# Performance work log

Hardware: AMD Instinct MI355X
Metric: run time of the kernel (lower is better)

Reference implementation:

```python
import jax, jax.numpy as jnp
import numpy as np

N, E = 50000, 800000
F_IN, HID, HEADS, NCLS = 128, 64, 4, 16
NEG_SLOPE = 0.2


def setup_inputs() -> dict:
    key = jax.random.key(0)
    ks = jax.random.split(key, 16)
    def glorot(k, shape):
        fan_in, fan_out = shape[0], shape[-1]
        lim = jnp.sqrt(6.0 / (fan_in + fan_out))
        return jax.random.uniform(k, shape, jnp.float32, -lim, lim)
    x = jax.random.normal(ks[0], (N, F_IN), jnp.float32)
    edge_index = jax.random.randint(ks[1], (2, E), 0, N, dtype=jnp.int64)
    inp = {"x": x, "edge_index": edge_index}
    # layer 1: F_IN -> HID x HEADS (concat)
    inp["W1"] = glorot(ks[2], (F_IN, HEADS * HID))
    inp["a1_src"] = glorot(ks[3], (HEADS, HID))
    inp["a1_dst"] = glorot(ks[4], (HEADS, HID))
    inp["b1"] = jnp.zeros((HEADS * HID,), jnp.float32)
    # layer 2: HEADS*HID -> HID x HEADS (concat)
    inp["W2"] = glorot(ks[5], (HEADS * HID, HEADS * HID))
    inp["a2_src"] = glorot(ks[6], (HEADS, HID))
    inp["a2_dst"] = glorot(ks[7], (HEADS, HID))
    inp["b2"] = jnp.zeros((HEADS * HID,), jnp.float32)
    # layer 3: HEADS*HID -> NCLS, heads=1, concat=False (mean)
    inp["W3"] = glorot(ks[8], (HEADS * HID, NCLS))
    inp["a3_src"] = glorot(ks[9], (1, NCLS))
    inp["a3_dst"] = glorot(ks[10], (1, NCLS))
    inp["b3"] = jnp.zeros((NCLS,), jnp.float32)
    return inp


def gat_conv(x, src, dst, W, a_src, a_dst, b, heads, out_dim, concat):
    n = x.shape[0]
    h = (x @ W).reshape(n, heads, out_dim)           # [N, H, D]
    s_src = jnp.sum(h * a_src, axis=-1)              # [N, H]
    s_dst = jnp.sum(h * a_dst, axis=-1)              # [N, H]
    e = jax.nn.leaky_relu(s_src[src] + s_dst[dst], NEG_SLOPE)  # [E, H]
    # segment softmax over incoming edges of each dst node
    m = jax.ops.segment_max(e, dst, num_segments=n)
    ex = jnp.exp(e - m[dst])
    z = jax.ops.segment_sum(ex, dst, num_segments=n)
    alpha = ex / z[dst]                              # [E, H]
    msg = h[src] * alpha[:, :, None]                 # [E, H, D]
    out = jax.ops.segment_sum(msg, dst, num_segments=n)  # [N, H, D]
    out = out.reshape(n, heads * out_dim) if concat else out.mean(axis=1)
    return out + b


def reference(x, edge_index, W1, a1_src, a1_dst, b1, W2, a2_src, a2_dst, b2,
              W3, a3_src, a3_dst, b3):
    n = x.shape[0]
    loop = jnp.arange(n, dtype=edge_index.dtype)
    src = jnp.concatenate([edge_index[0], loop])     # add self-loops (PyG default)
    dst = jnp.concatenate([edge_index[1], loop])
    h = jax.nn.elu(gat_conv(x, src, dst, W1, a1_src, a1_dst, b1, HEADS, HID, True))
    h = jax.nn.elu(gat_conv(h, src, dst, W2, a2_src, a2_dst, b2, HEADS, HID, True))
    h = gat_conv(h, src, dst, W3, a3_src, a3_dst, b3, 1, NCLS, False)
    return jax.nn.log_softmax(h, axis=1)
```

## Files before the change

kernel.cpp:

```cpp
#include <hip/hip_runtime.h>
#include <hip/hip_bf16.h>
#include <math.h>

#define N_NODES 50000
#define N_EDGES 800000
#define F_IN    128
#define HID     64
#define HEADS   4
#define NCLS    16
#define NEG_SLOPE 0.2f

typedef __attribute__((ext_vector_type(8))) _Float16 half8v;
typedef __attribute__((ext_vector_type(4))) float f32x4;
typedef __attribute__((ext_vector_type(2))) float f32x2;

static __device__ __forceinline__ float lrelu(float x) {
    return x >= 0.f ? x : NEG_SLOPE * x;
}
static __device__ __forceinline__ unsigned short f2h(float f) {
    _Float16 h = (_Float16)f;
    return __builtin_bit_cast(unsigned short, h);
}
static __device__ __forceinline__ float h2f(unsigned short u) {
    return (float)__builtin_bit_cast(_Float16, u);
}

__global__ void k_zero(int4* __restrict__ p, int n4) {
    int i = blockIdx.x * blockDim.x + threadIdx.x;
    if (i < n4) p[i] = int4{0, 0, 0, 0};
}

#define NB_WT1  128
#define NB_WT2  256
#define NB_HIST 3125
__global__ void k_prep(const float* __restrict__ W1, unsigned short* __restrict__ W1t,
                       const float* __restrict__ W2, unsigned short* __restrict__ W2t,
                       const int* __restrict__ dst, int* __restrict__ counts,
                       unsigned short* __restrict__ rank) {
    int bid = blockIdx.x, tid = threadIdx.x;
    if (bid < NB_WT1) {
        int i = bid * 256 + tid;
        int k = i >> 8, c = i & 255;
        W1t[c * F_IN + k] = f2h(W1[i]);
    } else if (bid < NB_WT1 + NB_WT2) {
        int i = (bid - NB_WT1) * 256 + tid;
        int k = i >> 8, c = i & 255;
        W2t[c * 256 + k] = f2h(W2[i]);
    } else {
        int i = (bid - NB_WT1 - NB_WT2) * 256 + tid;
        if (i < N_EDGES) rank[i] = (unsigned short)atomicAdd(&counts[dst[i]], 1);
    }
}

__global__ __launch_bounds__(256) void k_scan1(const int* __restrict__ counts, int* __restrict__ incl,
                                               int* __restrict__ bsums, int n) {
    __shared__ int wsum[4];
    int blk = blockIdx.x, tid = threadIdx.x;
    int lane = tid & 63, w = tid >> 6;
    int i0 = blk * 1024 + tid * 4;
    int v[4];
    #pragma unroll
    for (int j = 0; j < 4; j++) v[j] = (i0 + j < n) ? counts[i0 + j] : 0;
    int t = v[0] + v[1] + v[2] + v[3];
    int x = t;
    #pragma unroll
    for (int d = 1; d < 64; d <<= 1) { int y = __shfl_up(x, d); if (lane >= d) x += y; }
    if (lane == 63) wsum[w] = x;
    __syncthreads();
    int woff = 0;
    #pragma unroll
    for (int ww = 0; ww < 4; ww++) woff += (ww < w) ? wsum[ww] : 0;
    int p = woff + x - t;
    #pragma unroll
    for (int j = 0; j < 4; j++) { p += v[j]; if (i0 + j < n) incl[i0 + j] = p; }
    if (tid == 255) bsums[blk] = woff + x;
}

__global__ void k_scan2(const int* __restrict__ bsums, int* __restrict__ boffs, int nb, int* rowptr_end) {
    int lane = threadIdx.x;
    int v = (lane < nb) ? bsums[lane] : 0;
    int x = v;
    #pragma unroll
    for (int d = 1; d < 64; d <<= 1) { int y = __shfl_up(x, d); if (lane >= d) x += y; }
    if (lane < nb) boffs[lane] = x - v;
    if (lane == 63) *rowptr_end = x;
}

__global__ void k_scan3(const int* __restrict__ incl, const int* __restrict__ counts,
                        const int* __restrict__ boffs, int* __restrict__ rowptr, int n) {
    int i = blockIdx.x * blockDim.x + threadIdx.x;
    if (i < n) rowptr[i] = boffs[i >> 10] + incl[i] - counts[i];
}

static __device__ __forceinline__ int swz(int r, int lc) {
    return r * 4 + (lc ^ (r & 3) ^ ((r >> 2) & 1));
}

template<int CONVA>
static __device__ __forceinline__ void gemm_body(
        int bid, const void* __restrict__ Av, const unsigned short* __restrict__ Bt,
        const float* __restrict__ asrc, const float* __restrict__ adst,
        unsigned char* __restrict__ C8, float* __restrict__ s_src, float* __restrict__ s_dst,
        int M, int K, unsigned short* Asm, unsigned short* Bsm) {
    int tid = threadIdx.x;
    int lane = tid & 63, wid = tid >> 6;
    int bx = bid & 1, by = bid >> 1;
    int row0 = by * 128, col0 = bx * 128;
    int wr = wid >> 1, wc = wid & 1;
    f32x4 acc[4][4] = {};

    for (int k0 = 0; k0 < K; k0 += 32) {
        __syncthreads();
        #pragma unroll
        for (int s = 0; s < 2; s++) {
            int c = tid + s * 256;
            int row = c >> 2, lc = c & 3;
            int gr = row0 + row; if (gr >= M) gr = 0;
            uint4 va;
            if (CONVA) {
                const float* Af = (const float*)Av + (size_t)gr * K + k0 + lc * 8;
                float4 fa = *(const float4*)Af;
                float4 fb = *(const float4*)(Af + 4);
                va.x = (unsigned)f2h(fa.x) | ((unsigned)f2h(fa.y) << 16);
                va.y = (unsigned)f2h(fa.z) | ((unsigned)f2h(fa.w) << 16);
                va.z = (unsigned)f2h(fb.x) | ((unsigned)f2h(fb.y) << 16);
                va.w = (unsigned)f2h(fb.z) | ((unsigned)f2h(fb.w) << 16);
            } else {
                va = *(const uint4*)((const unsigned short*)Av + (size_t)gr * K + k0 + lc * 8);
            }
            *(uint4*)(&Asm[swz(row, lc) * 8]) = va;
            uint4 vb = *(const uint4*)(Bt + (size_t)(col0 + row) * K + k0 + lc * 8);
            *(uint4*)(&Bsm[swz(row, lc) * 8]) = vb;
        }
        __syncthreads();
        half8v af[4], bg[4];
        int lq = lane >> 4;
        #pragma unroll
        for (int m = 0; m < 4; m++) {
            int r = wr * 64 + m * 16 + (lane & 15);
            af[m] = *(const half8v*)(&Asm[swz(r, lq) * 8]);
        }
        #pragma unroll
        for (int n = 0; n < 4; n++) {
            int r = wc * 64 + n * 16 + (lane & 15);
            bg[n] = *(const half8v*)(&Bsm[swz(r, lq) * 8]);
        }
        #pragma unroll
        for (int m = 0; m < 4; m++)
            #pragma unroll
            for (int n = 0; n < 4; n++)
                acc[m][n] = __builtin_amdgcn_mfma_f32_16x16x32_f16(af[m], bg[n], acc[m][n], 0, 0, 0);
    }

    #pragma unroll
    for (int m = 0; m < 4; m++) {
        #pragma unroll
        for (int r = 0; r < 4; r++) {
            int row = row0 + wr * 64 + m * 16 + (lane >> 4) * 4 + r;
            if (row < M) {
                int q01 = __builtin_amdgcn_cvt_pk_fp8_f32(acc[m][0][r], acc[m][1][r], 0, false);
                int q23 = __builtin_amdgcn_cvt_pk_fp8_f32(acc[m][2][r], acc[m][3][r], 0, false);
                size_t base = (size_t)row * 256 + col0 + wc * 64 + (lane & 15);
                C8[base]      = (unsigned char)(q01 & 0xff);
                C8[base + 16] = (unsigned char)((q01 >> 8) & 0xff);
                C8[base + 32] = (unsigned char)(q23 & 0xff);
                C8[base + 48] = (unsigned char)((q23 >> 8) & 0xff);
            }
        }
    }

    int c16 = lane & 15, lq = lane >> 4;
    int head = bx * 2 + wc;
    float avs[4], avd[4];
    #pragma unroll
    for (int nn = 0; nn < 4; nn++) {
        avs[nn] = asrc[head * 64 + nn * 16 + c16];
        avd[nn] = adst[head * 64 + nn * 16 + c16];
    }
    #pragma unroll
    for (int mm = 0; mm < 4; mm++) {
        #pragma unroll
        for (int r = 0; r < 4; r++) {
            float ps = 0.f, pd = 0.f;
            #pragma unroll
            for (int nn = 0; nn < 4; nn++) {
                ps += acc[mm][nn][r] * avs[nn];
                pd += acc[mm][nn][r] * avd[nn];
            }
            #pragma unroll
            for (int off = 1; off < 16; off <<= 1) {
                ps += __shfl_xor(ps, off);
                pd += __shfl_xor(pd, off);
            }
            if (c16 == 0) {
                int grow = row0 + wr * 64 + mm * 16 + lq * 4 + r;
                if (grow < M) {
                    s_src[grow * 4 + head] = ps;
                    s_dst[grow * 4 + head] = pd;
                }
            }
        }
    }
}

__global__ __launch_bounds__(256) void k_gemm_mfma(const unsigned short* __restrict__ A,
                                                   const unsigned short* __restrict__ Bt,
                                                   const float* __restrict__ asrc,
                                                   const float* __restrict__ adst,
                                                   unsigned char* __restrict__ C8,
                                                   float* __restrict__ s_src,
                                                   float* __restrict__ s_dst,
                                                   int M, int K) {
    __shared__ unsigned short Asm[128 * 32];
    __shared__ unsigned short Bsm[128 * 32];
    gemm_body<0>(blockIdx.x, A, Bt, asrc, adst, C8, s_src, s_dst, M, K, Asm, Bsm);
}

__global__ __launch_bounds__(256) void k_b(const float* __restrict__ A,
                                           const unsigned short* __restrict__ Bt,
                                           const float* __restrict__ asrc,
                                           const float* __restrict__ adst,
                                           unsigned char* __restrict__ C8,
                                           float* __restrict__ s_src,
                                           float* __restrict__ s_dst,
                                           int M, int K, int gemmBlocks,
                                           const int* __restrict__ src, const int* __restrict__ dst,
                                           const int* __restrict__ rowptr,
                                           const unsigned short* __restrict__ rank,
                                           unsigned short* __restrict__ col, int e) {
    __shared__ unsigned short Asm[128 * 32];
    __shared__ unsigned short Bsm[128 * 32];
    int bid = blockIdx.x;
    if (bid < gemmBlocks) {
        gemm_body<1>(bid, A, Bt, asrc, adst, C8, s_src, s_dst, M, K, Asm, Bsm);
    } else {
        int half = (e + 1) >> 1;
        int i = (bid - gemmBlocks) * 256 + (int)threadIdx.x;
        if (i < half) {
            int d = dst[i];
            col[rowptr[d] + rank[i]] = (unsigned short)src[i];
        }
        int j = i + half;
        if (j < e) {
            int d = dst[j];
            col[rowptr[d] + rank[j]] = (unsigned short)src[j];
        }
    }
}

__global__ void k_aggregate(const unsigned char* __restrict__ h8, const int* __restrict__ rowptr,
                            const unsigned short* __restrict__ col,
                            const float* __restrict__ s_src, const float* __restrict__ s_dst,
                            const float* __restrict__ bias,
                            unsigned short* __restrict__ out, int n) {
    int wave = (blockIdx.x * blockDim.x + threadIdx.x) >> 6;
    int lane = threadIdx.x & 63;
    int half = lane >> 5, l5 = lane & 31;
    int node = wave * 2 + half;
    if (node >= n) return;
    int head = l5 >> 3;
    int j8 = l5 & 7;
    int base8 = lane & ~7;
    unsigned foff = (unsigned)(l5 * 8);
    int rs = rowptr[node], re = rowptr[node + 1];
    float sd = s_dst[node * 4 + head];

    float z = 0.f;
    f32x2 a01 = {0.f, 0.f}, a23 = {0.f, 0.f}, a45 = {0.f, 0.f}, a67 = {0.f, 0.f};
    #define PEDGE(SV) __expf(fminf(lrelu((SV) + sd), 80.f))
    #define ACC8(P, HV) { \
        f32x2 pbc = {(P), (P)}; \
        f32x2 v0 = __builtin_amdgcn_cvt_pk_f32_fp8((HV).x, false); \
        f32x2 v1 = __builtin_amdgcn_cvt_pk_f32_fp8((HV).x, true);  \
        f32x2 v2 = __builtin_amdgcn_cvt_pk_f32_fp8((HV).y, false); \
        f32x2 v3 = __builtin_amdgcn_cvt_pk_f32_fp8((HV).y, true);  \
        asm("v_pk_fma_f32 %0, %1, %2, %0" : "+v"(a01) : "v"(v0), "v"(pbc)); \
        asm("v_pk_fma_f32 %0, %1, %2, %0" : "+v"(a23) : "v"(v1), "v"(pbc)); \
        asm("v_pk_fma_f32 %0, %1, %2, %0" : "+v"(a45) : "v"(v2), "v"(pbc)); \
        asm("v_pk_fma_f32 %0, %1, %2, %0" : "+v"(a67) : "v"(v3), "v"(pbc)); \
        z += (P); }

    {
        float pself = PEDGE(s_src[node * 4 + head]);
        uint2 own = *(const uint2*)(h8 + (((unsigned)node << 8) + foff));
        ACC8(pself, own);
    }
    int i = rs;
    for (; i + 7 < re; i += 8) {
        unsigned cc[8];
        #pragma unroll
        for (int j = 0; j < 8; j++) cc[j] = col[i + j];
        float s_own = s_src[cc[j8] * 4 + head];
        uint2 hv[8];
        #pragma unroll
        for (int j = 0; j < 8; j++)
            hv[j] = *(const uint2*)(h8 + ((cc[j] << 8) + foff));
        float p_own = PEDGE(s_own);
        float pv[8];
        #pragma unroll
        for (int j = 0; j < 8; j++) pv[j] = __shfl(p_own, base8 + j);
        #pragma unroll
        for (int j = 0; j < 8; j++) { ACC8(pv[j], hv[j]); }
    }
    for (; i + 3 < re; i += 4) {
        unsigned cc[4];
        #pragma unroll
        for (int j = 0; j < 4; j++) cc[j] = col[i + j];
        float s_own = s_src[cc[j8 & 3] * 4 + head];
        uint2 hv[4];
        #pragma unroll
        for (int j = 0; j < 4; j++)
            hv[j] = *(const uint2*)(h8 + ((cc[j] << 8) + foff));
        float p_own = PEDGE(s_own);
        float pv[4];
        #pragma unroll
        for (int j = 0; j < 4; j++) pv[j] = __shfl(p_own, base8 + j);
        #pragma unroll
        for (int j = 0; j < 4; j++) { ACC8(pv[j], hv[j]); }
    }
    for (; i < re; i++) {
        unsigned c0 = col[i];
        float s0 = s_src[c0 * 4 + head];
        uint2 h0 = *(const uint2*)(h8 + ((c0 << 8) + foff));
        float p0 = PEDGE(s0);
        ACC8(p0, h0);
    }
    #undef ACC8
    #undef PEDGE

    float inv = 1.f / z;
    int f0 = l5 * 8;
    float4 bv0 = *(const float4*)(bias + f0);
    float4 bv1 = *(const float4*)(bias + f0 + 4);
    float o[8];
    o[0] = a01.x * inv + bv0.x; o[1] = a01.y * inv + bv0.y;
    o[2] = a23.x * inv + bv0.z; o[3] = a23.y * inv + bv0.w;
    o[4] = a45.x * inv + bv1.x; o[5] = a45.y * inv + bv1.y;
    o[6] = a67.x * inv + bv1.z; o[7] = a67.y * inv + bv1.w;
    #pragma unroll
    for (int j = 0; j < 8; j++) o[j] = o[j] > 0.f ? o[j] : __expf(o[j]) - 1.f;
    uint4 ov;
    unsigned* w = (unsigned*)&ov;
    #pragma unroll
    for (int j = 0; j < 4; j++)
        w[j] = (unsigned)f2h(o[2 * j]) | ((unsigned)f2h(o[2 * j + 1]) << 16);
    *(uint4*)(out + (size_t)node * 256 + f0) = ov;
}

__global__ __launch_bounds__(256) void k_gemm3(const unsigned short* __restrict__ A,
                                               const float* __restrict__ B,
                                               const float* __restrict__ a3s,
                                               const float* __restrict__ a3d,
                                               unsigned short* __restrict__ C,
                                               float* __restrict__ s_src,
                                               float* __restrict__ s_dst,
                                               int M, int K) {
    __shared__ float Bs[256 * 16];
    for (int i = threadIdx.x; i < K * 16; i += 256) Bs[i] = B[i];
    __syncthreads();
    int tx = threadIdx.x & 15;
    int ty = threadIdx.x >> 4;
    int row = blockIdx.x * 16 + ty;
    if (row >= M) return;
    const unsigned short* Ar = A + (size_t)row * K;
    float acc = 0.f;
    for (int kk = 0; kk < K; kk += 8) {
        uint4 va = *(const uint4*)(Ar + kk);
        const unsigned* u = (const unsigned*)&va;
        #pragma unroll
        for (int j = 0; j < 4; j++) {
            float lo = h2f((unsigned short)(u[j] & 0xffff));
            float hi = h2f((unsigned short)(u[j] >> 16));
            acc += lo * Bs[(kk + 2 * j) * 16 + tx] + hi * Bs[(kk + 2 * j + 1) * 16 + tx];
        }
    }
    C[(size_t)row * 16 + tx] = f2h(acc);
    float ps = acc * a3s[tx], pd = acc * a3d[tx];
    #pragma unroll
    for (int off = 1; off < 16; off <<= 1) {
        ps += __shfl_xor(ps, off);
        pd += __shfl_xor(pd, off);
    }
    if (tx == 0) { s_src[row] = ps; s_dst[row] = pd; }
}

__global__ void k_agg3(const unsigned short* __restrict__ h3, const int* __restrict__ rowptr,
                       const unsigned short* __restrict__ col,
                       const float* __restrict__ s_src, const float* __restrict__ s_dst,
                       const float* __restrict__ b3,
                       float* __restrict__ outp, int n) {
    int wave = (blockIdx.x * blockDim.x + threadIdx.x) >> 6;
    int lane = threadIdx.x & 63;
    if (wave >= n) return;
    int g = lane >> 4, c = lane & 15;
    int gbase = lane & ~15;
    int rs = rowptr[wave], re = rowptr[wave + 1];
    float sdn = s_dst[wave];

    float z = 0.f, acc = 0.f;
    if (g == 0) {
        float p = __expf(fminf(lrelu(s_src[wave] + sdn), 80.f));
        z += p;
        acc += p * h2f(h3[(size_t)wave * 16 + c]);
    }
    int i = rs + g;
    for (; i + 12 < re; i += 16) {
        int ss[4];
        #pragma unroll
        for (int j = 0; j < 4; j++) ss[j] = col[i + 4 * j];
        float q_own = s_src[ss[c & 3]];
        float v0 = h2f(h3[(size_t)ss[0] * 16 + c]), v1 = h2f(h3[(size_t)ss[1] * 16 + c]);
        float v2 = h2f(h3[(size_t)ss[2] * 16 + c]), v3 = h2f(h3[(size_t)ss[3] * 16 + c]);
        float p_own = __expf(fminf(lrelu(q_own + sdn), 80.f));
        float p0 = __shfl(p_own, gbase + 0);
        float p1 = __shfl(p_own, gbase + 1);
        float p2 = __shfl(p_own, gbase + 2);
        float p3 = __shfl(p_own, gbase + 3);
        z += (p0 + p1) + (p2 + p3);
        acc += p0 * v0 + p1 * v1 + p2 * v2 + p3 * v3;
    }
    for (; i < re; i += 4) {
        int s = col[i];
        float p = __expf(fminf(lrelu(s_src[s] + sdn), 80.f));
        z += p;
        acc += p * h2f(h3[(size_t)s * 16 + c]);
    }
    z += __shfl_xor(z, 16);  z += __shfl_xor(z, 32);
    acc += __shfl_xor(acc, 16); acc += __shfl_xor(acc, 32);
    if (lane < 16) {
        float v = acc / z + b3[c];
        float mm = v;
        #pragma unroll
        for (int off = 1; off < 16; off <<= 1) mm = fmaxf(mm, __shfl_xor(mm, off));
        float se = __expf(v - mm);
        #pragma unroll
        for (int off = 1; off < 16; off <<= 1) se += __shfl_xor(se, off);
        outp[(size_t)wave * 16 + c] = v - mm - logf(se);
    }
}

extern "C" void kernel_launch(void* const* d_in, const int* in_sizes, int n_in,
                              void* d_out, int out_size, void* d_ws, size_t ws_size,
                              hipStream_t stream) {
    const float* x      = (const float*)d_in[0];
    const int*   ei     = (const int*)d_in[1];
    const float* W1     = (const float*)d_in[2];
    const float* a1_src = (const float*)d_in[3];
    const float* a1_dst = (const float*)d_in[4];
    const float* b1     = (const float*)d_in[5];
    const float* W2     = (const float*)d_in[6];
    const float* a2_src = (const float*)d_in[7];
    const float* a2_dst = (const float*)d_in[8];
    const float* b2     = (const float*)d_in[9];
    const float* W3     = (const float*)d_in[10];
    const float* a3_src = (const float*)d_in[11];
    const float* a3_dst = (const float*)d_in[12];
    const float* b3     = (const float*)d_in[13];
    float* outp = (float*)d_out;

    const int N = N_NODES, E = N_EDGES;
    const int* src = ei;
    const int* dst = ei + E;

    char* ws = (char*)d_ws;
    size_t off = 0;
    auto alloc = [&](size_t bytes) {
        void* p = ws + off;
        off = (off + bytes + 255) & ~(size_t)255;
        return p;
    };
    int*   rowptr = (int*)alloc((N + 1) * sizeof(int));
    int*   counts = (int*)alloc(N * sizeof(int));
    unsigned short* col = (unsigned short*)alloc(E * sizeof(short));
    unsigned short* rank = (unsigned short*)alloc(E * sizeof(short));
    int*   incl   = (int*)alloc(N * sizeof(int));
    int*   bsums  = (int*)alloc(64 * sizeof(int));
    int*   boffs  = (int*)alloc(64 * sizeof(int));
    float* s_src  = (float*)alloc((size_t)N * HEADS * sizeof(float));
    float* s_dst  = (float*)alloc((size_t)N * HEADS * sizeof(float));
    unsigned short* W1t = (unsigned short*)alloc((size_t)256 * F_IN * sizeof(short));
    unsigned short* W2t = (unsigned short*)alloc((size_t)256 * 256 * sizeof(short));
    unsigned char* hA8  = (unsigned char*)alloc((size_t)N * 256);
    unsigned short* hB  = (unsigned short*)alloc((size_t)N * 256 * sizeof(short));
    unsigned short* h3  = (unsigned short*)alloc((size_t)N * 16 * sizeof(short));
    (void)ws_size;

    const int aggBlocks  = (N + 3) / 4;
    const int aggBlocks2 = (N + 7) / 8;
    const int gemmBlocks = ((N + 127) / 128) * 2;
    const int scatBlocks = ((E + 1) / 2 + 255) / 256;

    k_zero<<<(N / 4 + 255) / 256, 256, 0, stream>>>((int4*)counts, N / 4);
    k_prep<<<NB_WT1 + NB_WT2 + NB_HIST, 256, 0, stream>>>(W1, W1t, W2, W2t, dst, counts, rank);

    const int nb = (N + 1023) / 1024;
    k_scan1<<<nb, 256, 0, stream>>>(counts, incl, bsums, N);
    k_scan2<<<1, 64, 0, stream>>>(bsums, boffs, nb, rowptr + N);
    k_scan3<<<(N + 255) / 256, 256, 0, stream>>>(incl, counts, boffs, rowptr, N);

    k_b<<<gemmBlocks + scatBlocks, 256, 0, stream>>>(x, W1t, a1_src, a1_dst, hA8, s_src, s_dst,
                                                     N, F_IN, gemmBlocks,
                                                     src, dst, rowptr, rank, col, E);
    k_aggregate<<<aggBlocks2, 256, 0, stream>>>(hA8, rowptr, col, s_src, s_dst, b1, hB, N);
    k_gemm_mfma<<<gemmBlocks, 256, 0, stream>>>(hB, W2t, a2_src, a2_dst, hA8, s_src, s_dst, N, 256);
    k_aggregate<<<aggBlocks2, 256, 0, stream>>>(hA8, rowptr, col, s_src, s_dst, b2, hB, N);
    k_gemm3<<<(N + 15) / 16, 256, 0, stream>>>(hB, W3, a3_src, a3_dst, h3, s_src, s_dst, N, 256);
    k_agg3<<<aggBlocks, 256, 0, stream>>>(h3, rowptr, col, s_src, s_dst, b3, outp, N);
}
```

Baseline: 222.1 us.

## Fuse layer-1 aggregation with layer-2 GEMM via LDS-resident tile

Replaces the layer-1 aggregate kernel and the layer-2 MFMA GEMM with one kernel. Each 512-thread block aggregates 64 nodes into an fp16 tile held in LDS, then multiplies it by W2 and writes fp8 features plus attention scores to new buffers. This removes the round trip of the fp16 hidden activations through global memory and one launch. In exchange it uses a smaller GEMM tile, reloads W2 for every block, and needs 48KB of LDS, which may limit occupancy during the latency-bound gather phase.

```diff
diff --git a/kernel.cpp b/kernel.cpp
--- a/kernel.cpp
+++ b/kernel.cpp
@@ -201,19 +201,6 @@
             }
         }
     }
-}
-
-__global__ __launch_bounds__(256) void k_gemm_mfma(const unsigned short* __restrict__ A,
-                                                   const unsigned short* __restrict__ Bt,
-                                                   const float* __restrict__ asrc,
-                                                   const float* __restrict__ adst,
-                                                   unsigned char* __restrict__ C8,
-                                                   float* __restrict__ s_src,
-                                                   float* __restrict__ s_dst,
-                                                   int M, int K) {
-    __shared__ unsigned short Asm[128 * 32];
-    __shared__ unsigned short Bsm[128 * 32];
-    gemm_body<0>(blockIdx.x, A, Bt, asrc, adst, C8, s_src, s_dst, M, K, Asm, Bsm);
 }
 
 __global__ __launch_bounds__(256) void k_b(const float* __restrict__ A,
@@ -248,6 +235,199 @@
     }
 }
 
+#define PEDGE(SV, SD) __expf(fminf(lrelu((SV) + (SD)), 80.f))
+#define ACC8(P, HV) { \
+    f32x2 pbc = {(P), (P)}; \
+    f32x2 v0 = __builtin_amdgcn_cvt_pk_f32_fp8((HV).x, false); \
+    f32x2 v1 = __builtin_amdgcn_cvt_pk_f32_fp8((HV).x, true);  \
+    f32x2 v2 = __builtin_amdgcn_cvt_pk_f32_fp8((HV).y, false); \
+    f32x2 v3 = __builtin_amdgcn_cvt_pk_f32_fp8((HV).y, true);  \
+    asm("v_pk_fma_f32 %0, %1, %2, %0" : "+v"(a01) : "v"(v0), "v"(pbc)); \
+    asm("v_pk_fma_f32 %0, %1, %2, %0" : "+v"(a23) : "v"(v1), "v"(pbc)); \
+    asm("v_pk_fma_f32 %0, %1, %2, %0" : "+v"(a45) : "v"(v2), "v"(pbc)); \
+    asm("v_pk_fma_f32 %0, %1, %2, %0" : "+v"(a67) : "v"(v3), "v"(pbc)); \
+    z += (P); }
+
+__global__ __launch_bounds__(512) void k_fuse(
+        const unsigned char* __restrict__ h8, const int* __restrict__ rowptr,
+        const unsigned short* __restrict__ col,
+        const float* __restrict__ s_src, const float* __restrict__ s_dst,
+        const float* __restrict__ bias,
+        const unsigned short* __restrict__ Bt,
+        const float* __restrict__ asrc, const float* __restrict__ adst,
+        unsigned char* __restrict__ C8,
+        float* __restrict__ s_src2, float* __restrict__ s_dst2, int n) {
+    __shared__ unsigned short ALds[8 * 2048];
+    __shared__ unsigned short Bsm[8192];
+    int tid = threadIdx.x;
+    int lane = tid & 63, w = tid >> 6;
+    int blk = blockIdx.x;
+    int half = lane >> 5, l5 = lane & 31;
+    int head = l5 >> 3;
+    int j8 = l5 & 7;
+    int base8 = lane & ~7;
+    unsigned foff = (unsigned)(l5 * 8);
+
+    for (int pass = 0; pass < 4; pass++) {
+        int nl = w * 8 + pass * 2 + half;
+        int node = blk * 64 + nl;
+        uint4 ov = {0, 0, 0, 0};
+        if (node < n) {
+            int rs = rowptr[node], re = rowptr[node + 1];
+            float sd = s_dst[node * 4 + head];
+            float z = 0.f;
+            f32x2 a01 = {0.f, 0.f}, a23 = {0.f, 0.f}, a45 = {0.f, 0.f}, a67 = {0.f, 0.f};
+            {
+                float pself = PEDGE(s_src[node * 4 + head], sd);
+                uint2 own = *(const uint2*)(h8 + (((unsigned)node << 8) + foff));
+                ACC8(pself, own);
+            }
+            int i = rs;
+            for (; i + 7 < re; i += 8) {
+                unsigned cc[8];
+                #pragma unroll
+                for (int j = 0; j < 8; j++) cc[j] = col[i + j];
+                float s_own = s_src[cc[j8] * 4 + head];
+                uint2 hv[8];
+                #pragma unroll
+                for (int j = 0; j < 8; j++)
+                    hv[j] = *(const uint2*)(h8 + ((cc[j] << 8) + foff));
+                float p_own = PEDGE(s_own, sd);
+                float pv[8];
+                #pragma unroll
+                for (int j = 0; j < 8; j++) pv[j] = __shfl(p_own, base8 + j);
+                #pragma unroll
+                for (int j = 0; j < 8; j++) { ACC8(pv[j], hv[j]); }
+            }
+            for (; i + 3 < re; i += 4) {
+                unsigned cc[4];
+                #pragma unroll
+                for (int j = 0; j < 4; j++) cc[j] = col[i + j];
+                float s_own = s_src[cc[j8 & 3] * 4 + head];
+                uint2 hv[4];
+                #pragma unroll
+                for (int j = 0; j < 4; j++)
+                    hv[j] = *(const uint2*)(h8 + ((cc[j] << 8) + foff));
+                float p_own = PEDGE(s_own, sd);
+                float pv[4];
+                #pragma unroll
+                for (int j = 0; j < 4; j++) pv[j] = __shfl(p_own, base8 + j);
+                #pragma unroll
+                for (int j = 0; j < 4; j++) { ACC8(pv[j], hv[j]); }
+            }
+            for (; i < re; i++) {
+                unsigned c0 = col[i];
+                float s0 = s_src[c0 * 4 + head];
+                uint2 h0 = *(const uint2*)(h8 + ((c0 << 8) + foff));
+                float p0 = PEDGE(s0, sd);
+                ACC8(p0, h0);
+            }
+            float inv = 1.f / z;
+            int f0 = l5 * 8;
+            float4 bv0 = *(const float4*)(bias + f0);
+            float4 bv1 = *(const float4*)(bias + f0 + 4);
+            float o[8];
+            o[0] = a01.x * inv + bv0.x; o[1] = a01.y * inv + bv0.y;
+            o[2] = a23.x * inv + bv0.z; o[3] = a23.y * inv + bv0.w;
+            o[4] = a45.x * inv + bv1.x; o[5] = a45.y * inv + bv1.y;
+            o[6] = a67.x * inv + bv1.z; o[7] = a67.y * inv + bv1.w;
+            #pragma unroll
+            for (int j = 0; j < 8; j++) o[j] = o[j] > 0.f ? o[j] : __expf(o[j]) - 1.f;
+            unsigned* wd = (unsigned*)&ov;
+            #pragma unroll
+            for (int j = 0; j < 4; j++)
+                wd[j] = (unsigned)f2h(o[2 * j]) | ((unsigned)f2h(o[2 * j + 1]) << 16);
+        }
+        *(uint4*)(&ALds[(l5 >> 2) * 2048 + swz(nl, l5 & 3) * 8]) = ov;
+    }
+    __syncthreads();
+
+    f32x4 acc[2][4] = {};
+    int c16 = lane & 15, lq = lane >> 4;
+    int rw = (w >> 2) * 32;
+    int cw = (w & 3) * 64;
+    for (int ks = 0; ks < 8; ks++) {
+        {
+            int c = tid >> 1;
+            int lc0 = (tid & 1) * 2;
+            #pragma unroll
+            for (int q = 0; q < 2; q++) {
+                int lc = lc0 + q;
+                uint4 vb = *(const uint4*)(Bt + (size_t)c * 256 + ks * 32 + lc * 8);
+                *(uint4*)(&Bsm[swz(c, lc) * 8]) = vb;
+            }
+        }
+        __syncthreads();
+        half8v af[2], bg[4];
+        #pragma unroll
+        for (int m = 0; m < 2; m++) {
+            int r = rw + m * 16 + c16;
+            af[m] = *(const half8v*)(&ALds[ks * 2048 + swz(r, lq) * 8]);
+        }
+        #pragma unroll
+        for (int nn = 0; nn < 4; nn++) {
+            int c = cw + nn * 16 + c16;
+            bg[nn] = *(const half8v*)(&Bsm[swz(c, lq) * 8]);
+        }
+        #pragma unroll
+        for (int m = 0; m < 2; m++)
+            #pragma unroll
+            for (int nn = 0; nn < 4; nn++)
+                acc[m][nn] = __builtin_amdgcn_mfma_f32_16x16x32_f16(af[m], bg[nn], acc[m][nn], 0, 0, 0);
+        __syncthreads();
+    }
+
+    #pragma unroll
+    for (int m = 0; m < 2; m++) {
+        #pragma unroll
+        for (int r = 0; r < 4; r++) {
+            int row = blk * 64 + rw + m * 16 + lq * 4 + r;
+            if (row < n) {
+                int q01 = __builtin_amdgcn_cvt_pk_fp8_f32(acc[m][0][r], acc[m][1][r], 0, false);
+                int q23 = __builtin_amdgcn_cvt_pk_fp8_f32(acc[m][2][r], acc[m][3][r], 0, false);
+                size_t base = (size_t)row * 256 + cw + c16;
+                C8[base]      = (unsigned char)(q01 & 0xff);
+                C8[base + 16] = (unsigned char)((q01 >> 8) & 0xff);
+                C8[base + 32] = (unsigned char)(q23 & 0xff);
+                C8[base + 48] = (unsigned char)((q23 >> 8) & 0xff);
+            }
+        }
+    }
+    {
+        int head2 = w & 3;
+        float avs[4], avd[4];
+        #pragma unroll
+        for (int nn = 0; nn < 4; nn++) {
+            avs[nn] = asrc[head2 * 64 + nn * 16 + c16];
+            avd[nn] = adst[head2 * 64 + nn * 16 + c16];
+        }
+        #pragma unroll
+        for (int mm = 0; mm < 2; mm++) {
+            #pragma unroll
+            for (int r = 0; r < 4; r++) {
+                float ps = 0.f, pd = 0.f;
+                #pragma unroll
+                for (int nn = 0; nn < 4; nn++) {
+                    ps += acc[mm][nn][r] * avs[nn];
+                    pd += acc[mm][nn][r] * avd[nn];
+                }
+                #pragma unroll
+                for (int off = 1; off < 16; off <<= 1) {
+                    ps += __shfl_xor(ps, off);
+                    pd += __shfl_xor(pd, off);
+                }
+                if (c16 == 0) {
+                    int grow = blk * 64 + rw + mm * 16 + lq * 4 + r;
+                    if (grow < n) {
+                        s_src2[grow * 4 + head2] = ps;
+                        s_dst2[grow * 4 + head2] = pd;
+                    }
+                }
+            }
+        }
+    }
+}
+
 __global__ void k_aggregate(const unsigned char* __restrict__ h8, const int* __restrict__ rowptr,
                             const unsigned short* __restrict__ col,
                             const float* __restrict__ s_src, const float* __restrict__ s_dst,
@@ -267,21 +447,8 @@
 
     float z = 0.f;
     f32x2 a01 = {0.f, 0.f}, a23 = {0.f, 0.f}, a45 = {0.f, 0.f}, a67 = {0.f, 0.f};
-    #define PEDGE(SV) __expf(fminf(lrelu((SV) + sd), 80.f))
-    #define ACC8(P, HV) { \
-        f32x2 pbc = {(P), (P)}; \
-        f32x2 v0 = __builtin_amdgcn_cvt_pk_f32_fp8((HV).x, false); \
-        f32x2 v1 = __builtin_amdgcn_cvt_pk_f32_fp8((HV).x, true);  \
-        f32x2 v2 = __builtin_amdgcn_cvt_pk_f32_fp8((HV).y, false); \
-        f32x2 v3 = __builtin_amdgcn_cvt_pk_f32_fp8((HV).y, true);  \
-        asm("v_pk_fma_f32 %0, %1, %2, %0" : "+v"(a01) : "v"(v0), "v"(pbc)); \
-        asm("v_pk_fma_f32 %0, %1, %2, %0" : "+v"(a23) : "v"(v1), "v"(pbc)); \
-        asm("v_pk_fma_f32 %0, %1, %2, %0" : "+v"(a45) : "v"(v2), "v"(pbc)); \
-        asm("v_pk_fma_f32 %0, %1, %2, %0" : "+v"(a67) : "v"(v3), "v"(pbc)); \
-        z += (P); }
-
     {
-        float pself = PEDGE(s_src[node * 4 + head]);
+        float pself = PEDGE(s_src[node * 4 + head], sd);
         uint2 own = *(const uint2*)(h8 + (((unsigned)node << 8) + foff));
         ACC8(pself, own);
     }
@@ -295,7 +462,7 @@
         #pragma unroll
         for (int j = 0; j < 8; j++)
             hv[j] = *(const uint2*)(h8 + ((cc[j] << 8) + foff));
-        float p_own = PEDGE(s_own);
+        float p_own = PEDGE(s_own, sd);
         float pv[8];
         #pragma unroll
         for (int j = 0; j < 8; j++) pv[j] = __shfl(p_own, base8 + j);
@@ -311,7 +478,7 @@
         #pragma unroll
         for (int j = 0; j < 4; j++)
             hv[j] = *(const uint2*)(h8 + ((cc[j] << 8) + foff));
-        float p_own = PEDGE(s_own);
+        float p_own = PEDGE(s_own, sd);
         float pv[4];
         #pragma unroll
         for (int j = 0; j < 4; j++) pv[j] = __shfl(p_own, base8 + j);
@@ -322,11 +489,9 @@
         unsigned c0 = col[i];
         float s0 = s_src[c0 * 4 + head];
         uint2 h0 = *(const uint2*)(h8 + ((c0 << 8) + foff));
-        float p0 = PEDGE(s0);
+        float p0 = PEDGE(s0, sd);
         ACC8(p0, h0);
     }
-    #undef ACC8
-    #undef PEDGE
 
     float inv = 1.f / z;
     int f0 = l5 * 8;
@@ -340,10 +505,10 @@
     #pragma unroll
     for (int j = 0; j < 8; j++) o[j] = o[j] > 0.f ? o[j] : __expf(o[j]) - 1.f;
     uint4 ov;
-    unsigned* w = (unsigned*)&ov;
+    unsigned* wd = (unsigned*)&ov;
     #pragma unroll
     for (int j = 0; j < 4; j++)
-        w[j] = (unsigned)f2h(o[2 * j]) | ((unsigned)f2h(o[2 * j + 1]) << 16);
+        wd[j] = (unsigned)f2h(o[2 * j]) | ((unsigned)f2h(o[2 * j + 1]) << 16);
     *(uint4*)(out + (size_t)node * 256 + f0) = ov;
 }
 
@@ -478,9 +643,12 @@
     int*   boffs  = (int*)alloc(64 * sizeof(int));
     float* s_src  = (float*)alloc((size_t)N * HEADS * sizeof(float));
     float* s_dst  = (float*)alloc((size_t)N * HEADS * sizeof(float));
+    float* s_src2 = (float*)alloc((size_t)N * HEADS * sizeof(float));
+    float* s_dst2 = (float*)alloc((size_t)N * HEADS * sizeof(float));
     unsigned short* W1t = (unsigned short*)alloc((size_t)256 * F_IN * sizeof(short));
     unsigned short* W2t = (unsigned short*)alloc((size_t)256 * 256 * sizeof(short));
     unsigned char* hA8  = (unsigned char*)alloc((size_t)N * 256);
+    unsigned char* hB8  = (unsigned char*)alloc((size_t)N * 256);
     unsigned short* hB  = (unsigned short*)alloc((size_t)N * 256 * sizeof(short));
     unsigned short* h3  = (unsigned short*)alloc((size_t)N * 16 * sizeof(short));
     (void)ws_size;
@@ -488,6 +656,7 @@
     const int aggBlocks  = (N + 3) / 4;
     const int aggBlocks2 = (N + 7) / 8;
     const int gemmBlocks = ((N + 127) / 128) * 2;
+    const int fuseBlocks = (N + 63) / 64;
     const int scatBlocks = ((E + 1) / 2 + 255) / 256;
 
     k_zero<<<(N / 4 + 255) / 256, 256, 0, stream>>>((int4*)counts, N / 4);
@@ -501,9 +670,9 @@
     k_b<<<gemmBlocks + scatBlocks, 256, 0, stream>>>(x, W1t, a1_src, a1_dst, hA8, s_src, s_dst,
                                                      N, F_IN, gemmBlocks,
                                                      src, dst, rowptr, rank, col, E);
-    k_aggregate<<<aggBlocks2, 256, 0, stream>>>(hA8, rowptr, col, s_src, s_dst, b1, hB, N);
-    k_gemm_mfma<<<gemmBlocks, 256, 0, stream>>>(hB, W2t, a2_src, a2_dst, hA8, s_src, s_dst, N, 256);
-    k_aggregate<<<aggBlocks2, 256, 0, stream>>>(hA8, rowptr, col, s_src, s_dst, b2, hB, N);
+    k_fuse<<<fuseBlocks, 512, 0, stream>>>(hA8, rowptr, col, s_src, s_dst, b1,
+                                           W2t, a2_src, a2_dst, hB8, s_src2, s_dst2, N);
+    k_aggregate<<<aggBlocks2, 256, 0, stream>>>(hB8, rowptr, col, s_src2, s_dst2, b2, hB, N);
     k_gemm3<<<(N + 15) / 16, 256, 0, stream>>>(hB, W3, a3_src, a3_dst, h3, s_src, s_dst, N, 256);
     k_agg3<<<aggBlocks, 256, 0, stream>>>(h3, rowptr, col, s_src, s_dst, b3, outp, N);
 }
```

Result: slower. 226.7 us (+2.1%).

## Fuse layer-3 projection GEMM into layer-2 aggregation epilogue via MFMA

Applied to the files above, without the earlier changes.

The layer-2 aggregation now writes each block's 8 aggregated rows to LDS, and one wave multiplies them by a pre-transposed fp16 W3 with an MFMA 16x16x32 instruction. It then emits h3 and the layer-3 attention scores directly. This removes the separate k_gemm3 launch and the full write and re-read of the N×256 fp16 hB tensor. In exchange it adds a barrier and serialises the small GEMM onto one wave per block, using only half of each MFMA tile. W3 is transposed to fp16 inside the prep kernel, and separate s_src3/s_dst3 buffers are added.

```diff
diff --git a/kernel.cpp b/kernel.cpp
--- a/kernel.cpp
+++ b/kernel.cpp
@@ -32,9 +32,11 @@
 
 #define NB_WT1  128
 #define NB_WT2  256
+#define NB_WT3  16
 #define NB_HIST 3125
 __global__ void k_prep(const float* __restrict__ W1, unsigned short* __restrict__ W1t,
                        const float* __restrict__ W2, unsigned short* __restrict__ W2t,
+                       const float* __restrict__ W3, unsigned short* __restrict__ W3ht,
                        const int* __restrict__ dst, int* __restrict__ counts,
                        unsigned short* __restrict__ rank) {
     int bid = blockIdx.x, tid = threadIdx.x;
@@ -46,8 +48,12 @@
         int i = (bid - NB_WT1) * 256 + tid;
         int k = i >> 8, c = i & 255;
         W2t[c * 256 + k] = f2h(W2[i]);
+    } else if (bid < NB_WT1 + NB_WT2 + NB_WT3) {
+        int i = (bid - NB_WT1 - NB_WT2) * 256 + tid;
+        int k = i >> 4, c = i & 15;
+        W3ht[c * 256 + k] = f2h(W3[i]);
     } else {
-        int i = (bid - NB_WT1 - NB_WT2) * 256 + tid;
+        int i = (bid - NB_WT1 - NB_WT2 - NB_WT3) * 256 + tid;
         if (i < N_EDGES) rank[i] = (unsigned short)atomicAdd(&counts[dst[i]], 1);
     }
 }
@@ -248,6 +254,94 @@
     }
 }
 
+#define PEDGE(SV, SD) __expf(fminf(lrelu((SV) + (SD)), 80.f))
+#define ACC8(P, HV) { \
+    f32x2 pbc = {(P), (P)}; \
+    f32x2 v0 = __builtin_amdgcn_cvt_pk_f32_fp8((HV).x, false); \
+    f32x2 v1 = __builtin_amdgcn_cvt_pk_f32_fp8((HV).x, true);  \
+    f32x2 v2 = __builtin_amdgcn_cvt_pk_f32_fp8((HV).y, false); \
+    f32x2 v3 = __builtin_amdgcn_cvt_pk_f32_fp8((HV).y, true);  \
+    asm("v_pk_fma_f32 %0, %1, %2, %0" : "+v"(a01) : "v"(v0), "v"(pbc)); \
+    asm("v_pk_fma_f32 %0, %1, %2, %0" : "+v"(a23) : "v"(v1), "v"(pbc)); \
+    asm("v_pk_fma_f32 %0, %1, %2, %0" : "+v"(a45) : "v"(v2), "v"(pbc)); \
+    asm("v_pk_fma_f32 %0, %1, %2, %0" : "+v"(a67) : "v"(v3), "v"(pbc)); \
+    z += (P); }
+
+static __device__ __forceinline__ uint4 agg_core(
+        int node, int n, int head, int j8, int base8, unsigned foff,
+        const unsigned char* __restrict__ h8, const int* __restrict__ rowptr,
+        const unsigned short* __restrict__ col,
+        const float* __restrict__ s_src, const float* __restrict__ s_dst,
+        const float* __restrict__ bias, int l5) {
+    uint4 ov = {0, 0, 0, 0};
+    if (node >= n) return ov;
+    int rs = rowptr[node], re = rowptr[node + 1];
+    float sd = s_dst[node * 4 + head];
+    float z = 0.f;
+    f32x2 a01 = {0.f, 0.f}, a23 = {0.f, 0.f}, a45 = {0.f, 0.f}, a67 = {0.f, 0.f};
+    {
+        float pself = PEDGE(s_src[node * 4 + head], sd);
+        uint2 own = *(const uint2*)(h8 + (((unsigned)node << 8) + foff));
+        ACC8(pself, own);
+    }
+    int i = rs;
+    for (; i + 7 < re; i += 8) {
+        unsigned cc[8];
+        #pragma unroll
+        for (int j = 0; j < 8; j++) cc[j] = col[i + j];
+        float s_own = s_src[cc[j8] * 4 + head];
+        uint2 hv[8];
+        #pragma unroll
+        for (int j = 0; j < 8; j++)
+            hv[j] = *(const uint2*)(h8 + ((cc[j] << 8) + foff));
+        float p_own = PEDGE(s_own, sd);
+        float pv[8];
+        #pragma unroll
+        for (int j = 0; j < 8; j++) pv[j] = __shfl(p_own, base8 + j);
+        #pragma unroll
+        for (int j = 0; j < 8; j++) { ACC8(pv[j], hv[j]); }
+    }
+    for (; i + 3 < re; i += 4) {
+        unsigned cc[4];
+        #pragma unroll
+        for (int j = 0; j < 4; j++) cc[j] = col[i + j];
+        float s_own = s_src[cc[j8 & 3] * 4 + head];
+        uint2 hv[4];
+        #pragma unroll
+        for (int j = 0; j < 4; j++)
+            hv[j] = *(const uint2*)(h8 + ((cc[j] << 8) + foff));
+        float p_own = PEDGE(s_own, sd);
+        float pv[4];
+        #pragma unroll
+        for (int j = 0; j < 4; j++) pv[j] = __shfl(p_own, base8 + j);
+        #pragma unroll
+        for (int j = 0; j < 4; j++) { ACC8(pv[j], hv[j]); }
+    }
+    for (; i < re; i++) {
+        unsigned c0 = col[i];
+        float s0 = s_src[c0 * 4 + head];
+        uint2 h0 = *(const uint2*)(h8 + ((c0 << 8) + foff));
+        float p0 = PEDGE(s0, sd);
+        ACC8(p0, h0);
+    }
+    float inv = 1.f / z;
+    int f0 = l5 * 8;
+    float4 bv0 = *(const float4*)(bias + f0);
+    float4 bv1 = *(const float4*)(bias + f0 + 4);
+    float o[8];
+    o[0] = a01.x * inv + bv0.x; o[1] = a01.y * inv + bv0.y;
+    o[2] = a23.x * inv + bv0.z; o[3] = a23.y * inv + bv0.w;
+    o[4] = a45.x * inv + bv1.x; o[5] = a45.y * inv + bv1.y;
+    o[6] = a67.x * inv + bv1.z; o[7] = a67.y * inv + bv1.w;
+    #pragma unroll
+    for (int j = 0; j < 8; j++) o[j] = o[j] > 0.f ? o[j] : __expf(o[j]) - 1.f;
+    unsigned* wd = (unsigned*)&ov;
+    #pragma unroll
+    for (int j = 0; j < 4; j++)
+        wd[j] = (unsigned)f2h(o[2 * j]) | ((unsigned)f2h(o[2 * j + 1]) << 16);
+    return ov;
+}
+
 __global__ void k_aggregate(const unsigned char* __restrict__ h8, const int* __restrict__ rowptr,
                             const unsigned short* __restrict__ col,
                             const float* __restrict__ s_src, const float* __restrict__ s_dst,
@@ -262,126 +356,62 @@
     int j8 = l5 & 7;
     int base8 = lane & ~7;
     unsigned foff = (unsigned)(l5 * 8);
-    int rs = rowptr[node], re = rowptr[node + 1];
-    float sd = s_dst[node * 4 + head];
-
-    float z = 0.f;
-    f32x2 a01 = {0.f, 0.f}, a23 = {0.f, 0.f}, a45 = {0.f, 0.f}, a67 = {0.f, 0.f};
-    #define PEDGE(SV) __expf(fminf(lrelu((SV) + sd), 80.f))
-    #define ACC8(P, HV) { \
-        f32x2 pbc = {(P), (P)}; \
-        f32x2 v0 = __builtin_amdgcn_cvt_pk_f32_fp8((HV).x, false); \
-        f32x2 v1 = __builtin_amdgcn_cvt_pk_f32_fp8((HV).x, true);  \
-        f32x2 v2 = __builtin_amdgcn_cvt_pk_f32_fp8((HV).y, false); \
-        f32x2 v3 = __builtin_amdgcn_cvt_pk_f32_fp8((HV).y, true);  \
-        asm("v_pk_fma_f32 %0, %1, %2, %0" : "+v"(a01) : "v"(v0), "v"(pbc)); \
-        asm("v_pk_fma_f32 %0, %1, %2, %0" : "+v"(a23) : "v"(v1), "v"(pbc)); \
-        asm("v_pk_fma_f32 %0, %1, %2, %0" : "+v"(a45) : "v"(v2), "v"(pbc)); \
-        asm("v_pk_fma_f32 %0, %1, %2, %0" : "+v"(a67) : "v"(v3), "v"(pbc)); \
-        z += (P); }
-
-    {
-        float pself = PEDGE(s_src[node * 4 + head]);
-        uint2 own = *(const uint2*)(h8 + (((unsigned)node << 8) + foff));
-        ACC8(pself, own);
-    }
-    int i = rs;
-    for (; i + 7 < re; i += 8) {
-        unsigned cc[8];
-        #pragma unroll
-        for (int j = 0; j < 8; j++) cc[j] = col[i + j];
-        float s_own = s_src[cc[j8] * 4 + head];
-        uint2 hv[8];
-        #pragma unroll
-        for (int j = 0; j < 8; j++)
-            hv[j] = *(const uint2*)(h8 + ((cc[j] << 8) + foff));
-        float p_own = PEDGE(s_own);
-        float pv[8];
-        #pragma unroll
-        for (int j = 0; j < 8; j++) pv[j] = __shfl(p_own, base8 + j);
-        #pragma unroll
-        for (int j = 0; j < 8; j++) { ACC8(pv[j], hv[j]); }
-    }
-    for (; i + 3 < re; i += 4) {
-        unsigned cc[4];
-        #pragma unroll
-        for (int j = 0; j < 4; j++) cc[j] = col[i + j];
-        float s_own = s_src[cc[j8 & 3] * 4 + head];
-        uint2 hv[4];
-        #pragma unroll
-        for (int j = 0; j < 4; j++)
-            hv[j] = *(const uint2*)(h8 + ((cc[j] << 8) + foff));
-        float p_own = PEDGE(s_own);
-        float pv[4];
-        #pragma unroll
-        for (int j = 0; j < 4; j++) pv[j] = __shfl(p_own, base8 + j);
-        #pragma unroll
-        for (int j = 0; j < 4; j++) { ACC8(pv[j], hv[j]); }
-    }
-    for (; i < re; i++) {
-        unsigned c0 = col[i];
-        float s0 = s_src[c0 * 4 + head];
-        uint2 h0 = *(const uint2*)(h8 + ((c0 << 8) + foff));
-        float p0 = PEDGE(s0);
-        ACC8(p0, h0);
-    }
-    #undef ACC8
-    #undef PEDGE
-
-    float inv = 1.f / z;
-    int f0 = l5 * 8;
-    float4 bv0 = *(const float4*)(bias + f0);
-    float4 bv1 = *(const float4*)(bias + f0 + 4);
-    float o[8];
-    o[0] = a01.x * inv + bv0.x; o[1] = a01.y * inv + bv0.y;
-    o[2] = a23.x * inv + bv0.z; o[3] = a23.y * inv + bv0.w;
-    o[4] = a45.x * inv + bv1.x; o[5] = a45.y * inv + bv1.y;
-    o[6] = a67.x * inv + bv1.z; o[7] = a67.y * inv + bv1.w;
-    #pragma unroll
-    for (int j = 0; j < 8; j++) o[j] = o[j] > 0.f ? o[j] : __expf(o[j]) - 1.f;
-    uint4 ov;
-    unsigned* w = (unsigned*)&ov;
-    #pragma unroll
-    for (int j = 0; j < 4; j++)
-        w[j] = (unsigned)f2h(o[2 * j]) | ((unsigned)f2h(o[2 * j + 1]) << 16);
-    *(uint4*)(out + (size_t)node * 256 + f0) = ov;
-}
-
-__global__ __launch_bounds__(256) void k_gemm3(const unsigned short* __restrict__ A,
-                                               const float* __restrict__ B,
-                                               const float* __restrict__ a3s,
-                                               const float* __restrict__ a3d,
-                                               unsigned short* __restrict__ C,
-                                               float* __restrict__ s_src,
-                                               float* __restrict__ s_dst,
-                                               int M, int K) {
-    __shared__ float Bs[256 * 16];
-    for (int i = threadIdx.x; i < K * 16; i += 256) Bs[i] = B[i];
+    uint4 ov = agg_core(node, n, head, j8, base8, foff, h8, rowptr, col, s_src, s_dst, bias, l5);
+    *(uint4*)(out + (size_t)node * 256 + l5 * 8) = ov;
+}
+
+__global__ __launch_bounds__(256) void k_agg2(
+        const unsigned char* __restrict__ h8, const int* __restrict__ rowptr,
+        const unsigned short* __restrict__ col,
+        const float* __restrict__ s_src, const float* __restrict__ s_dst,
+        const float* __restrict__ bias,
+        const unsigned short* __restrict__ W3ht,
+        const float* __restrict__ a3s, const float* __restrict__ a3d,
+        unsigned short* __restrict__ h3,
+        float* __restrict__ s_src3, float* __restrict__ s_dst3, int n) {
+    __shared__ unsigned short ALds[16 * 264];
+    int tid = threadIdx.x;
+    int lane = tid & 63, wv = tid >> 6;
+    int half = lane >> 5, l5 = lane & 31;
+    int nl = wv * 2 + half;
+    int node = blockIdx.x * 8 + nl;
+    for (int i = tid; i < (8 * 264) / 2; i += 256) ((unsigned*)&ALds[8 * 264])[i] = 0;
+
+    int head = l5 >> 3;
+    int j8 = l5 & 7;
+    int base8 = lane & ~7;
+    unsigned foff = (unsigned)(l5 * 8);
+    uint4 ov = agg_core(node, n, head, j8, base8, foff, h8, rowptr, col, s_src, s_dst, bias, l5);
+    *(uint4*)(&ALds[nl * 264 + l5 * 8]) = ov;
     __syncthreads();
-    int tx = threadIdx.x & 15;
-    int ty = threadIdx.x >> 4;
-    int row = blockIdx.x * 16 + ty;
-    if (row >= M) return;
-    const unsigned short* Ar = A + (size_t)row * K;
-    float acc = 0.f;
-    for (int kk = 0; kk < K; kk += 8) {
-        uint4 va = *(const uint4*)(Ar + kk);
-        const unsigned* u = (const unsigned*)&va;
-        #pragma unroll
-        for (int j = 0; j < 4; j++) {
-            float lo = h2f((unsigned short)(u[j] & 0xffff));
-            float hi = h2f((unsigned short)(u[j] >> 16));
-            acc += lo * Bs[(kk + 2 * j) * 16 + tx] + hi * Bs[(kk + 2 * j + 1) * 16 + tx];
-        }
-    }
-    C[(size_t)row * 16 + tx] = f2h(acc);
-    float ps = acc * a3s[tx], pd = acc * a3d[tx];
-    #pragma unroll
-    for (int off = 1; off < 16; off <<= 1) {
-        ps += __shfl_xor(ps, off);
-        pd += __shfl_xor(pd, off);
-    }
-    if (tx == 0) { s_src[row] = ps; s_dst[row] = pd; }
+
+    if (wv == 0) {
+        int col16 = lane & 15, lq = lane >> 4;
+        f32x4 acc3 = {0.f, 0.f, 0.f, 0.f};
+        #pragma unroll
+        for (int ks = 0; ks < 8; ks++) {
+            half8v af = *(const half8v*)(&ALds[col16 * 264 + ks * 32 + lq * 8]);
+            half8v bg = *(const half8v*)(W3ht + col16 * 256 + ks * 32 + lq * 8);
+            acc3 = __builtin_amdgcn_mfma_f32_16x16x32_f16(af, bg, acc3, 0, 0, 0);
+        }
+        float a3sv = a3s[col16], a3dv = a3d[col16];
+        #pragma unroll
+        for (int r = 0; r < 4; r++) {
+            int row = lq * 4 + r;
+            int gnode = blockIdx.x * 8 + row;
+            float v = acc3[r];
+            float ps = v * a3sv, pd = v * a3dv;
+            #pragma unroll
+            for (int off = 1; off < 16; off <<= 1) {
+                ps += __shfl_xor(ps, off);
+                pd += __shfl_xor(pd, off);
+            }
+            if (row < 8 && gnode < n) {
+                h3[(size_t)gnode * 16 + col16] = f2h(v);
+                if (col16 == 0) { s_src3[gnode] = ps; s_dst3[gnode] = pd; }
+            }
+        }
+    }
 }
 
 __global__ void k_agg3(const unsigned short* __restrict__ h3, const int* __restrict__ rowptr,
@@ -478,8 +508,11 @@
     int*   boffs  = (int*)alloc(64 * sizeof(int));
     float* s_src  = (float*)alloc((size_t)N * HEADS * sizeof(float));
     float* s_dst  = (float*)alloc((size_t)N * HEADS * sizeof(float));
+    float* s_src3 = (float*)alloc((size_t)N * sizeof(float));
+    float* s_dst3 = (float*)alloc((size_t)N * sizeof(float));
     unsigned short* W1t = (unsigned short*)alloc((size_t)256 * F_IN * sizeof(short));
     unsigned short* W2t = (unsigned short*)alloc((size_t)256 * 256 * sizeof(short));
+    unsigned short* W3ht = (unsigned short*)alloc((size_t)16 * 256 * sizeof(short));
     unsigned char* hA8  = (unsigned char*)alloc((size_t)N * 256);
     unsigned short* hB  = (unsigned short*)alloc((size_t)N * 256 * sizeof(short));
     unsigned short* h3  = (unsigned short*)alloc((size_t)N * 16 * sizeof(short));
@@ -491,7 +524,8 @@
     const int scatBlocks = ((E + 1) / 2 + 255) / 256;
 
     k_zero<<<(N / 4 + 255) / 256, 256, 0, stream>>>((int4*)counts, N / 4);
-    k_prep<<<NB_WT1 + NB_WT2 + NB_HIST, 256, 0, stream>>>(W1, W1t, W2, W2t, dst, counts, rank);
+    k_prep<<<NB_WT1 + NB_WT2 + NB_WT3 + NB_HIST, 256, 0, stream>>>(W1, W1t, W2, W2t, W3, W3ht,
+                                                                   dst, counts, rank);
 
     const int nb = (N + 1023) / 1024;
     k_scan1<<<nb, 256, 0, stream>>>(counts, incl, bsums, N);
@@ -503,7 +537,7 @@
                                                      src, dst, rowptr, rank, col, E);
     k_aggregate<<<aggBlocks2, 256, 0, stream>>>(hA8, rowptr, col, s_src, s_dst, b1, hB, N);
     k_gemm_mfma<<<gemmBlocks, 256, 0, stream>>>(hB, W2t, a2_src, a2_dst, hA8, s_src, s_dst, N, 256);
-    k_aggregate<<<aggBlocks2, 256, 0, stream>>>(hA8, rowptr, col, s_src, s_dst, b2, hB, N);
-    k_gemm3<<<(N + 15) / 16, 256, 0, stream>>>(hB, W3, a3_src, a3_dst, h3, s_src, s_dst, N, 256);
-    k_agg3<<<aggBlocks, 256, 0, stream>>>(h3, rowptr, col, s_src, s_dst, b3, outp, N);
-}
+    k_agg2<<<aggBlocks2, 256, 0, stream>>>(hA8, rowptr, col, s_src, s_dst, b2,
+                                           W3ht, a3_src, a3_dst, h3, s_src3, s_dst3, N);
+    k_agg3<<<aggBlocks, 256, 0, stream>>>(h3, rowptr, col, s_src3, s_dst3, b3, outp, N);
+}
```

After: 204.5 us (median of 3 runs). -7.9%, faster.
